# Performance work log

Hardware: AMD Instinct MI355X
Metric: run time of the kernel (lower is better)

Reference implementation:

```python
import jax, jax.numpy as jnp
import numpy as np

B, T, NIN, H = 256, 100, 64, 1024


def _lstm_cell(x, h, c, Wih, Whh, bih, bhh):
    # torch.nn.LSTMCell: gates = x@Wih^T + bih + h@Whh^T + bhh, order (i, f, g, o)
    gates = x @ Wih.T + bih + h @ Whh.T + bhh  # [B, 4H]
    i, f, g, o = jnp.split(gates, 4, axis=-1)
    i = jax.nn.sigmoid(i)
    f = jax.nn.sigmoid(f)
    g = jnp.tanh(g)
    o = jax.nn.sigmoid(o)
    c_new = f * c + i * g
    h_new = o * jnp.tanh(c_new)
    return h_new, c_new


def setup_inputs() -> dict:
    key = jax.random.key(0)
    ks = jax.random.split(key, 17)
    s_in = 1.0 / np.sqrt(H)
    d = {"x": jax.random.normal(ks[0], (B, T, NIN), dtype=jnp.float32)}
    dims_in = [NIN, H, H, H]
    ki = 1
    for layer in range(1, 5):
        din = dims_in[layer - 1]
        d[f"Wih{layer}"] = jax.random.normal(ks[ki], (4 * H, din), dtype=jnp.float32) * s_in; ki += 1
        d[f"Whh{layer}"] = jax.random.normal(ks[ki], (4 * H, H), dtype=jnp.float32) * s_in; ki += 1
        d[f"bih{layer}"] = jax.random.normal(ks[ki], (4 * H,), dtype=jnp.float32) * s_in; ki += 1
        d[f"bhh{layer}"] = jax.random.normal(ks[ki], (4 * H,), dtype=jnp.float32) * s_in; ki += 1
        ks = jax.random.split(ks[-1], 17)
        ki = 0
    return d


def reference(x, Wih1, Whh1, bih1, bhh1, Wih2, Whh2, bih2, bhh2,
              Wih3, Whh3, bih3, bhh3, Wih4, Whh4, bih4, bhh4):
    batch = x.shape[0]
    params = ((Wih1, Whh1, bih1, bhh1), (Wih2, Whh2, bih2, bhh2),
              (Wih3, Whh3, bih3, bhh3), (Wih4, Whh4, bih4, bhh4))
    zeros = jnp.zeros((batch, H), dtype=x.dtype)
    init = tuple((zeros, zeros) for _ in range(4))

    def step(carry, xt):
        new_carry = []
        inp = xt
        for (h, c), (Wih, Whh, bih, bhh) in zip(carry, params):
            h, c = _lstm_cell(inp, h, c, Wih, Whh, bih, bhh)
            new_carry.append((h, c))
            inp = h
        return tuple(new_carry), inp  # top-layer h

    xs = jnp.swapaxes(x, 0, 1)  # [T, B, NIN]
    carry, hs = jax.lax.scan(step, init, xs)
    out = jnp.swapaxes(hs, 0, 1)  # [B, T, H]
    c4 = carry[3][1]
    return out, c4
```

## Files before the change

### kernel.cpp

```cpp
#include <hip/hip_runtime.h>
#include <hip/hip_bf16.h>

typedef __hip_bfloat16 bf16;
typedef unsigned short u16;
typedef unsigned int u32;
typedef __attribute__((ext_vector_type(8))) short bf16x8;
typedef __attribute__((ext_vector_type(4))) float f32x4;

#define BATCH 256
#define TLEN 100
#define HDIM 1024
#define G4 4096
#define OUT_HT (BATCH * TLEN * HDIM)

#define WS_WP 0u
#define WS_BIAS 59244544u
#define WS_XT 59310080u
#define WS_H 62586880u
#define WS_BAR (WS_H + 4194304u)

__device__ __forceinline__ float sigm(float x) { return 1.0f / (1.0f + __expf(-x)); }
__device__ __forceinline__ float tanh_(float x) { return 2.0f / (1.0f + __expf(-2.0f * x)) - 1.0f; }

__device__ __forceinline__ void gl_lds16(const void* g, void* l) {
  __builtin_amdgcn_global_load_lds((const __attribute__((address_space(1))) u32*)g,
                                   (__attribute__((address_space(3))) u32*)l, 16, 0, 0);
}

__device__ __forceinline__ void gbar(u32* arrive, u32* release, u32 epoch, int tid) {
  __syncthreads();
  if (tid == 0) {
    u32 old = __hip_atomic_fetch_add(arrive, 1u, __ATOMIC_ACQ_REL, __HIP_MEMORY_SCOPE_AGENT);
    if (old == 255u) {
      __hip_atomic_store(arrive, 0u, __ATOMIC_RELAXED, __HIP_MEMORY_SCOPE_AGENT);
      __hip_atomic_store(release, epoch, __ATOMIC_RELEASE, __HIP_MEMORY_SCOPE_AGENT);
    } else {
      while (__hip_atomic_load(release, __ATOMIC_RELAXED, __HIP_MEMORY_SCOPE_AGENT) < epoch)
        __builtin_amdgcn_s_sleep(2);
      __builtin_amdgcn_fence(__ATOMIC_ACQUIRE, "agent");
    }
  }
  __syncthreads();
}


__global__ void pack_w(const float* __restrict__ wih, const float* __restrict__ whh,
                       bf16* __restrict__ dst, int NC, int din) {
  int i = blockIdx.x * 256 + threadIdx.x;
  if (i >= 32 * NC * 128 * 64) return;
  int k6 = i & 63;
  int r = (i >> 6) & 127;
  int jc = i >> 13;
  int c = jc % NC;
  int j = jc / NC;
  int grow = ((r >> 5) << 10) + j * 32 + (r & 31);
  int k = c * 64 + k6;
  float v = (k < din) ? wih[grow * din + k] : whh[(grow << 10) + (k - din)];
  dst[(jc << 13) + (r << 6) + (k6 ^ ((r & 7) << 3))] = __float2bfloat16(v);
}

__global__ void pack_bias(const float* __restrict__ a, const float* __restrict__ b,
                          float* __restrict__ dst) {
  int i = blockIdx.x * 256 + threadIdx.x;
  if (i < G4) dst[i] = a[i] + b[i];
}

__global__ void pack_x(const float* __restrict__ x, bf16* __restrict__ xT) {
  int i = blockIdx.x * 256 + threadIdx.x;
  if (i >= TLEN * BATCH * 64) return;
  int k = i & 63;
  int b = (i >> 6) & 255;
  int t = i >> 14;
  xT[(t << 14) + (b << 6) + (k ^ ((b & 7) << 3))] = __float2bfloat16(x[(b * TLEN + t) * 64 + k]);
}


__global__ void __launch_bounds__(512, 2)
lstm_main(const u16* __restrict__ Wp, const float* __restrict__ biasc,
          const u16* __restrict__ xT, u16* __restrict__ hbuf,
          float* __restrict__ out, u32* __restrict__ barr) {
  __shared__ __align__(16) u16 smem[73728];
  float* Gs = (float*)smem;

  const int tid = threadIdx.x;
  const int lane = tid & 63;
  const int wave = tid >> 6;
  const int wg = blockIdx.x;
  const int layer = wg >> 6;
  const int sub = wg & 63;
  const int b0 = (sub >> 5) * 128;
  const int h0 = (sub & 31) * 32;

  const int NC = (layer == 0) ? 17 : 32;
  const int T0 = (layer == 0) ? 1 : 16;
  const u16* Wsl = Wp + ((layer == 0) ? 0u : (4456448u + (u32)(layer - 1) * 8388608u))
                 + (u32)(sub & 31) * (u32)NC * 8192u;

  const int nn = tid & 31;
  float bias_r[4];
#pragma unroll
  for (int g = 0; g < 4; ++g) bias_r[g] = biasc[layer * G4 + g * HDIM + h0 + nn];

  const int r0 = (tid >> 5) * 8;
  float cst[8];
#pragma unroll
  for (int k = 0; k < 8; ++k) cst[k] = 0.0f;

  const int opu0 = (wave * 2) * 512 + lane * 8;
  const int opu1 = opu0 + 512;

  const int mb = (wave & 3) * 32;
  const int nbase = (wave >> 2) * 64;
  const int lrow = lane & 15;
  const int lcb0 = (lane >> 4) << 4;
  const int lswz = (lane & 7) << 4;

  u32* bar_arrive = barr;
  u32* bar_release = barr + 32;

  for (int s = 0; s < TLEN + 3; ++s) {
    const int t = s - layer;
    if (t >= 0 && t < TLEN) {
      const u16* aBase0 = ((layer == 0) ? (xT + (u32)t * 16384u)
                                        : (hbuf + (u32)((layer - 1) * 2 + (t & 1)) * 262144u))
                        + b0 * 64;
      const u16* aBase1 = hbuf + (u32)(layer * 2 + ((t + 1) & 1)) * 262144u + b0 * 64;

      f32x4 acc[2][4];
#pragma unroll
      for (int mt = 0; mt < 2; ++mt)
#pragma unroll
        for (int nt = 0; nt < 4; ++nt) acc[mt][nt] = (f32x4)(0.0f);

      auto issueA = [&](int c, int slot) {
        const u16* src = (c < T0) ? (aBase0 + c * 16384) : (aBase1 + (c - T0) * 16384);
        gl_lds16(src + opu0, smem + slot * 8192 + (wave * 2) * 512);
        gl_lds16(src + opu1, smem + slot * 8192 + (wave * 2 + 1) * 512);
      };
      auto issueB = [&](int c, int slot) {
        const u16* src = Wsl + c * 8192;
        gl_lds16(src + opu0, smem + 32768 + slot * 8192 + (wave * 2) * 512);
        gl_lds16(src + opu1, smem + 32768 + slot * 8192 + (wave * 2 + 1) * 512);
      };

      issueB(0, 0);
      issueB(1, 1);
      issueA(0, 0); issueB(2, 2);
      issueA(1, 1); issueB(3, 3);

      for (int c = 0; c < NC; ++c) {
        {
          int ca = c + 2; int cca = (ca < NC) ? ca : (NC - 1);
          issueA(cca, ca & 3);
          int cb = c + 4; int ccb = (cb < NC) ? cb : (NC - 1);
          issueB(ccb, cb % 5);
        }
        asm volatile("s_waitcnt vmcnt(10)" ::: "memory");
        __builtin_amdgcn_s_barrier();

        const char* Abuf = (const char*)smem + (c & 3) * 16384;
        const char* Bbuf = (const char*)smem + 65536 + (c % 5) * 16384;
        bf16x8 a[2][2], b[2][4];
#pragma unroll
        for (int ks = 0; ks < 2; ++ks) {
#pragma unroll
          for (int mt = 0; mt < 2; ++mt) {
            int row = mb + mt * 16 + lrow;
            a[ks][mt] = *(const bf16x8*)(Abuf + row * 128 + ((ks * 64 + lcb0) ^ lswz));
          }
#pragma unroll
          for (int nt = 0; nt < 4; ++nt) {
            int j = nbase + nt * 16 + lrow;
            b[ks][nt] = *(const bf16x8*)(Bbuf + j * 128 + ((ks * 64 + lcb0) ^ lswz));
          }
        }
#pragma unroll
        for (int ks = 0; ks < 2; ++ks)
#pragma unroll
          for (int mt = 0; mt < 2; ++mt)
#pragma unroll
            for (int nt = 0; nt < 4; ++nt)
              acc[mt][nt] = __builtin_amdgcn_mfma_f32_16x16x32_bf16(a[ks][mt], b[ks][nt], acc[mt][nt], 0, 0, 0);

        __builtin_amdgcn_s_barrier();
      }

      asm volatile("s_waitcnt vmcnt(0)" ::: "memory");
      __syncthreads();

#pragma unroll
      for (int mt = 0; mt < 2; ++mt)
#pragma unroll
        for (int nt = 0; nt < 4; ++nt) {
          int row = mb + mt * 16 + (lane >> 4) * 4;
          int col = nbase + nt * 16 + (lane & 15);
#pragma unroll
          for (int r = 0; r < 4; ++r) Gs[(row + r) * 132 + col] = acc[mt][nt][r];
        }
      __syncthreads();

      u16* outSlot = hbuf + (u32)(layer * 2 + (t & 1)) * 262144u;
      const int hcol = h0 + nn;
      const int j2 = hcol >> 6;
      const int colin = hcol & 63;
#pragma unroll
      for (int k = 0; k < 8; ++k) {
        int r = r0 + k;
        float gi = Gs[r * 132 + nn] + bias_r[0];
        float gf = Gs[r * 132 + 32 + nn] + bias_r[1];
        float gg = Gs[r * 132 + 64 + nn] + bias_r[2];
        float go = Gs[r * 132 + 96 + nn] + bias_r[3];
        float iv = sigm(gi), fv = sigm(gf), gv = tanh_(gg), ov = sigm(go);
        float cv = fv * cst[k] + iv * gv;
        cst[k] = cv;
        float hv = ov * tanh_(cv);
        int b = b0 + r;
        bf16 hb = __float2bfloat16(hv);
        outSlot[j2 * 16384 + b * 64 + (colin ^ ((b & 7) << 3))] = *(u16*)&hb;
        if (layer == 3) {
          __builtin_nontemporal_store(hv, &out[((size_t)b * TLEN + t) * HDIM + hcol]);
          if (t == TLEN - 1)
            __builtin_nontemporal_store(cv, &out[OUT_HT + (size_t)b * HDIM + hcol]);
        }
      }
    }
    if (s < TLEN + 2) gbar(bar_arrive, bar_release, (u32)(s + 1), tid);
  }
}


extern "C" void kernel_launch(void* const* d_in, const int* in_sizes, int n_in,
                              void* d_out, int out_size, void* d_ws, size_t ws_size,
                              hipStream_t stream) {
  const float* x = (const float*)d_in[0];
  const float* Wih[4] = {(const float*)d_in[1], (const float*)d_in[5],
                         (const float*)d_in[9], (const float*)d_in[13]};
  const float* Whh[4] = {(const float*)d_in[2], (const float*)d_in[6],
                         (const float*)d_in[10], (const float*)d_in[14]};
  const float* bih[4] = {(const float*)d_in[3], (const float*)d_in[7],
                         (const float*)d_in[11], (const float*)d_in[15]};
  const float* bhh[4] = {(const float*)d_in[4], (const float*)d_in[8],
                         (const float*)d_in[12], (const float*)d_in[16]};

  char* ws = (char*)d_ws;
  bf16* Wp = (bf16*)(ws + WS_WP);
  float* biasc = (float*)(ws + WS_BIAS);
  bf16* xT = (bf16*)(ws + WS_XT);
  u16* hbuf = (u16*)(ws + WS_H);
  u32* barr = (u32*)(ws + WS_BAR);
  float* out = (float*)d_out;

  for (int l = 0; l < 4; ++l) {
    int NC = (l == 0) ? 17 : 32;
    int din = (l == 0) ? 64 : 1024;
    bf16* dst = Wp + ((l == 0) ? 0 : (4456448 + (size_t)(l - 1) * 8388608));
    int total = 32 * NC * 128 * 64;
    pack_w<<<(total + 255) / 256, 256, 0, stream>>>(Wih[l], Whh[l], dst, NC, din);
    pack_bias<<<16, 256, 0, stream>>>(bih[l], bhh[l], biasc + l * 4096);
  }
  pack_x<<<(TLEN * BATCH * 64 + 255) / 256, 256, 0, stream>>>(x, xT);
  hipMemsetAsync(ws + WS_H, 0, 4194304u + 256u, stream);

  void* args[] = {(void*)&Wp, (void*)&biasc, (void*)&xT, (void*)&hbuf, (void*)&out, (void*)&barr};
  hipLaunchCooperativeKernel((void*)lstm_main, dim3(256), dim3(512), args, 0, stream);
}
```

Measured before the change: 3.423 ms.

## Split K across wave pairs with 64x64 warp tiles and reduce in LDS

Each wave now owns a 64x64 output tile and half of each 64-wide K chunk, in place of a 32x64 tile over the full K chunk. Two waves write partial gate sums into separate LDS regions (G0, G1), and the epilogue adds them. This cuts LDS fragment reads per MFMA (8 loads feed 16 MFMAs) and raises register-level reuse, at the cost of more accumulator registers, a second LDS gate buffer, and an extra add in the epilogue. The output stores also switch from nontemporal to ordinary stores.

```diff
diff --git a/kernel.cpp b/kernel.cpp
--- a/kernel.cpp
+++ b/kernel.cpp
@@ -80,7 +80,6 @@
           const u16* __restrict__ xT, u16* __restrict__ hbuf,
           float* __restrict__ out, u32* __restrict__ barr) {
   __shared__ __align__(16) u16 smem[73728];
-  float* Gs = (float*)smem;
 
   const int tid = threadIdx.x;
   const int lane = tid & 63;
@@ -109,11 +108,16 @@
   const int opu0 = (wave * 2) * 512 + lane * 8;
   const int opu1 = opu0 + 512;
 
-  const int mb = (wave & 3) * 32;
-  const int nbase = (wave >> 2) * 64;
+  const int mh = (wave >> 2) & 1;
+  const int nh = (wave >> 1) & 1;
+  const int kh = wave & 1;
   const int lrow = lane & 15;
-  const int lcb0 = (lane >> 4) << 4;
   const int lswz = (lane & 7) << 4;
+  const int kbyte = kh * 64 + ((lane >> 4) << 4);
+  const int kx = kbyte ^ lswz;
+
+  float* G0 = (float*)smem;
+  float* G1 = (float*)((char*)smem + 67584);
 
   u32* bar_arrive = barr;
   u32* bar_release = barr + 32;
@@ -126,9 +130,9 @@
                         + b0 * 64;
       const u16* aBase1 = hbuf + (u32)(layer * 2 + ((t + 1) & 1)) * 262144u + b0 * 64;
 
-      f32x4 acc[2][4];
-#pragma unroll
-      for (int mt = 0; mt < 2; ++mt)
+      f32x4 acc[4][4];
+#pragma unroll
+      for (int mt = 0; mt < 4; ++mt)
 #pragma unroll
         for (int nt = 0; nt < 4; ++nt) acc[mt][nt] = (f32x4)(0.0f);
 
@@ -160,27 +164,22 @@
 
         const char* Abuf = (const char*)smem + (c & 3) * 16384;
         const char* Bbuf = (const char*)smem + 65536 + (c % 5) * 16384;
-        bf16x8 a[2][2], b[2][4];
-#pragma unroll
-        for (int ks = 0; ks < 2; ++ks) {
-#pragma unroll
-          for (int mt = 0; mt < 2; ++mt) {
-            int row = mb + mt * 16 + lrow;
-            a[ks][mt] = *(const bf16x8*)(Abuf + row * 128 + ((ks * 64 + lcb0) ^ lswz));
-          }
-#pragma unroll
-          for (int nt = 0; nt < 4; ++nt) {
-            int j = nbase + nt * 16 + lrow;
-            b[ks][nt] = *(const bf16x8*)(Bbuf + j * 128 + ((ks * 64 + lcb0) ^ lswz));
-          }
-        }
-#pragma unroll
-        for (int ks = 0; ks < 2; ++ks)
-#pragma unroll
-          for (int mt = 0; mt < 2; ++mt)
-#pragma unroll
-            for (int nt = 0; nt < 4; ++nt)
-              acc[mt][nt] = __builtin_amdgcn_mfma_f32_16x16x32_bf16(a[ks][mt], b[ks][nt], acc[mt][nt], 0, 0, 0);
+        bf16x8 a[4], b[4];
+#pragma unroll
+        for (int mt = 0; mt < 4; ++mt) {
+          int row = mh * 64 + mt * 16 + lrow;
+          a[mt] = *(const bf16x8*)(Abuf + row * 128 + kx);
+        }
+#pragma unroll
+        for (int nt = 0; nt < 4; ++nt) {
+          int row = nh * 64 + nt * 16 + lrow;
+          b[nt] = *(const bf16x8*)(Bbuf + row * 128 + kx);
+        }
+#pragma unroll
+        for (int mt = 0; mt < 4; ++mt)
+#pragma unroll
+          for (int nt = 0; nt < 4; ++nt)
+            acc[mt][nt] = __builtin_amdgcn_mfma_f32_16x16x32_bf16(a[mt], b[nt], acc[mt][nt], 0, 0, 0);
 
         __builtin_amdgcn_s_barrier();
       }
@@ -188,14 +187,15 @@
       asm volatile("s_waitcnt vmcnt(0)" ::: "memory");
       __syncthreads();
 
-#pragma unroll
-      for (int mt = 0; mt < 2; ++mt)
+      float* Gw = kh ? G1 : G0;
+#pragma unroll
+      for (int mt = 0; mt < 4; ++mt)
 #pragma unroll
         for (int nt = 0; nt < 4; ++nt) {
-          int row = mb + mt * 16 + (lane >> 4) * 4;
-          int col = nbase + nt * 16 + (lane & 15);
-#pragma unroll
-          for (int r = 0; r < 4; ++r) Gs[(row + r) * 132 + col] = acc[mt][nt][r];
+          int row = mh * 64 + mt * 16 + (lane >> 4) * 4;
+          int col = nh * 64 + nt * 16 + (lane & 15);
+#pragma unroll
+          for (int r = 0; r < 4; ++r) Gw[(row + r) * 132 + col] = acc[mt][nt][r];
         }
       __syncthreads();
 
@@ -206,10 +206,10 @@
 #pragma unroll
       for (int k = 0; k < 8; ++k) {
         int r = r0 + k;
-        float gi = Gs[r * 132 + nn] + bias_r[0];
-        float gf = Gs[r * 132 + 32 + nn] + bias_r[1];
-        float gg = Gs[r * 132 + 64 + nn] + bias_r[2];
-        float go = Gs[r * 132 + 96 + nn] + bias_r[3];
+        float gi = G0[r * 132 + nn]      + G1[r * 132 + nn]      + bias_r[0];
+        float gf = G0[r * 132 + 32 + nn] + G1[r * 132 + 32 + nn] + bias_r[1];
+        float gg = G0[r * 132 + 64 + nn] + G1[r * 132 + 64 + nn] + bias_r[2];
+        float go = G0[r * 132 + 96 + nn] + G1[r * 132 + 96 + nn] + bias_r[3];
         float iv = sigm(gi), fv = sigm(gf), gv = tanh_(gg), ov = sigm(go);
         float cv = fv * cst[k] + iv * gv;
         cst[k] = cv;
@@ -218,9 +218,8 @@
         bf16 hb = __float2bfloat16(hv);
         outSlot[j2 * 16384 + b * 64 + (colin ^ ((b & 7) << 3))] = *(u16*)&hb;
         if (layer == 3) {
-          __builtin_nontemporal_store(hv, &out[((size_t)b * TLEN + t) * HDIM + hcol]);
-          if (t == TLEN - 1)
-            __builtin_nontemporal_store(cv, &out[OUT_HT + (size_t)b * HDIM + hcol]);
+          out[((size_t)b * TLEN + t) * HDIM + hcol] = hv;
+          if (t == TLEN - 1) out[OUT_HT + (size_t)b * HDIM + hcol] = cv;
         }
       }
     }
```

Result: faster. 3.274 ms (-4.4%).
